# Optimization experiments

Hardware: AMD Instinct MI355X
Metric: run time of the kernel (lower is better)

## Reference

```python
import jax, jax.numpy as jnp
import numpy as np

N_HEADS = 8
N_HIDDEN = 64  # out_features // n_heads
SLOPE = 0.2
NEG = -9e15


def setup_inputs() -> dict:
    key = jax.random.key(0)
    k1, k2, k3, k4, k5 = jax.random.split(key, 5)
    B, N, F_in, F_out = 4, 2048, 512, 512
    h = jax.random.normal(k1, (B, N, F_in), dtype=jnp.float32)
    adj = jax.random.randint(k2, (B, N, N), 0, 2, dtype=jnp.int32)
    # xavier_uniform with gain=1.414: limit = gain*sqrt(6/(fan_in+fan_out))
    lim_W = 1.414 * np.sqrt(6.0 / (F_in + F_out))
    W_l = jax.random.uniform(k3, (F_in, F_out), jnp.float32, -lim_W, lim_W)
    W_r = jax.random.uniform(k4, (F_in, F_out), jnp.float32, -lim_W, lim_W)
    lim_a = 1.414 * np.sqrt(6.0 / (N_HIDDEN + 1))
    a = jax.random.uniform(k5, (N_HIDDEN, 1), jnp.float32, -lim_a, lim_a)
    return {"h": h, "adj": adj, "W_l": W_l, "W_r": W_r, "a": a}


def reference(h, adj, W_l, W_r, a):
    B, N, _ = h.shape
    H, d = N_HEADS, N_HIDDEN
    # torch .view(-1, H, N, d) is a raw row-major reshape, replicated exactly here
    Wh_l = jax.nn.leaky_relu((h @ W_l).reshape(B, H, N, d), SLOPE)
    Wh_r = jax.nn.leaky_relu((h @ W_r).reshape(B, H, N, d), SLOPE)
    # e: [B,H,N,1] + [B,H,1,N] -> [B,H,N,N]
    e = Wh_l @ a + jnp.swapaxes(Wh_r @ a, 2, 3)
    att = jnp.where(adj[:, None, :, :] > 0, e, NEG)
    att = jax.nn.softmax(att, axis=-1)
    h_prime = att @ Wh_r  # [B,H,N,d]
    # torch .view(-1, N, H*d): raw reshape (no head transpose)
    out = jax.nn.elu(h_prime.reshape(B, N, H * d))
    return out
```

## Files before the change

kernel.cpp:

```cpp
#include <hip/hip_runtime.h>

#define NB   4
#define NN   2048
#define FIN  512
#define FOUT 512
#define NHD  8
#define DH   64
#define VC   576
#define SLOPE 0.2f

typedef __attribute__((ext_vector_type(8)))  short bhalf8;
typedef __attribute__((ext_vector_type(16))) float f32x16;

__device__ __forceinline__ void load_lds16(const void* g, void* l) {
  __builtin_amdgcn_global_load_lds(
      (const __attribute__((address_space(1))) unsigned int*)g,
      (__attribute__((address_space(3))) unsigned int*)l, 16, 0, 0);
}

__device__ __forceinline__ unsigned int bfpair(float lo, float hi) {
  unsigned int a = __float_as_uint(lo), b = __float_as_uint(hi);
  a = (a + 0x7FFFu + ((a >> 16) & 1u)) >> 16;
  b = (b + 0x7FFFu + ((b >> 16) & 1u)) & 0xFFFF0000u;
  return a | b;
}

__device__ __forceinline__ void split2(float x, float y,
                                       unsigned int& hp, unsigned int& lp) {
  unsigned int ux = __float_as_uint(x), uy = __float_as_uint(y);
  unsigned int rx = (ux + 0x7FFFu + ((ux >> 16) & 1u)) & 0xFFFF0000u;
  unsigned int ry = (uy + 0x7FFFu + ((uy >> 16) & 1u)) & 0xFFFF0000u;
  float lx = x - __uint_as_float(rx);
  float ly = y - __uint_as_float(ry);
  unsigned int vx = __float_as_uint(lx), vy = __float_as_uint(ly);
  hp = (rx >> 16) | ry;
  lp = ((vx + 0x7FFFu + ((vx >> 16) & 1u)) >> 16)
     | ((vy + 0x7FFFu + ((vy >> 16) & 1u)) & 0xFFFF0000u);
}

__global__ __launch_bounds__(256) void k_split_h(
    const float* __restrict__ h,
    unsigned short* __restrict__ hHi, unsigned short* __restrict__ hLo)
{
  size_t base = ((size_t)blockIdx.x * 256 + threadIdx.x) * 8;
  float4 a = *(const float4*)(h + base);
  float4 b = *(const float4*)(h + base + 4);
  uint4 uh, ul;
  split2(a.x, a.y, uh.x, ul.x);
  split2(a.z, a.w, uh.y, ul.y);
  split2(b.x, b.y, uh.z, ul.z);
  split2(b.z, b.w, uh.w, ul.w);
  *(uint4*)(hHi + base) = uh;
  *(uint4*)(hLo + base) = ul;
}

__global__ __launch_bounds__(256) void k_prep_wr(
    const float* __restrict__ Wr,
    unsigned short* __restrict__ wTh, unsigned short* __restrict__ wTl)
{
  __shared__ float s[64][65];
  const int t = threadIdx.x;
  const int k0 = blockIdx.y * 64, n0 = blockIdx.x * 64;
#pragma unroll
  for (int p = 0; p < 4; ++p) {
    int row = p * 16 + (t >> 4);
    int col = (t & 15) * 4;
    float4 v = *(const float4*)(Wr + (size_t)(k0 + row) * FOUT + n0 + col);
    s[row][col] = v.x; s[row][col+1] = v.y; s[row][col+2] = v.z; s[row][col+3] = v.w;
  }
  __syncthreads();
  const int n = t >> 2;
  const int ks = (t & 3) * 16;
  uint4 h0, h1, l0, l1;
  split2(s[ks+ 0][n], s[ks+ 1][n], h0.x, l0.x);
  split2(s[ks+ 2][n], s[ks+ 3][n], h0.y, l0.y);
  split2(s[ks+ 4][n], s[ks+ 5][n], h0.z, l0.z);
  split2(s[ks+ 6][n], s[ks+ 7][n], h0.w, l0.w);
  split2(s[ks+ 8][n], s[ks+ 9][n], h1.x, l1.x);
  split2(s[ks+10][n], s[ks+11][n], h1.y, l1.y);
  split2(s[ks+12][n], s[ks+13][n], h1.z, l1.z);
  split2(s[ks+14][n], s[ks+15][n], h1.w, l1.w);
  size_t o = (size_t)(n0 + n) * FIN + k0 + ks;
  *(uint4*)(wTh + o) = h0; *(uint4*)(wTh + o + 8) = h1;
  *(uint4*)(wTl + o) = l0; *(uint4*)(wTl + o + 8) = l1;
}

__global__ __launch_bounds__(256) void k_gemm_whr_mfma(
    const unsigned short* __restrict__ hHi, const unsigned short* __restrict__ hLo,
    const unsigned short* __restrict__ wTh, const unsigned short* __restrict__ wTl,
    float* __restrict__ Whr)
{
  __shared__ unsigned short sAh[128*64], sAl[128*64];
  __shared__ unsigned short sBh[64*64],  sBl[64*64];
  const int tid = threadIdx.x, lane = tid & 63, wv = tid >> 6;
  const int Bid = blockIdx.x;
  const int g8 = Bid & 7, idx = Bid >> 3;
  const int sg = idx >> 3, ct = idx & 7;
  const int c0 = ct * 64;
  const int row0 = (g8 * 8 + sg) * 128;

  const unsigned short* pAh[4]; const unsigned short* pAl[4];
  unsigned short *dAh[4], *dAl[4];
#pragma unroll
  for (int t = 0; t < 4; ++t) {
    int I  = wv + t * 4;
    int rl = I * 8 + (lane >> 3);
    int gk = (lane & 7) ^ (rl & 7);
    pAh[t] = hHi + (size_t)(row0 + rl) * FIN + gk * 8;
    pAl[t] = hLo + (size_t)(row0 + rl) * FIN + gk * 8;
    dAh[t] = sAh + I * 512;  dAl[t] = sAl + I * 512;
  }
  const unsigned short* pBh[2]; const unsigned short* pBl[2];
  unsigned short *dBh[2], *dBl[2];
#pragma unroll
  for (int t = 0; t < 2; ++t) {
    int I  = wv + t * 4;
    int rl = I * 8 + (lane >> 3);
    int gk = (lane & 7) ^ (rl & 7);
    pBh[t] = wTh + (size_t)(c0 + rl) * FIN + gk * 8;
    pBl[t] = wTl + (size_t)(c0 + rl) * FIN + gk * 8;
    dBh[t] = sBh + I * 512;  dBl[t] = sBl + I * 512;
  }

  const int wi = wv >> 1, wc = wv & 1;
  const int l31 = lane & 31, half = lane >> 5;
  const int aoff0 = (wi*64 +      l31) * 64;
  const int aoff1 = (wi*64 + 32 + l31) * 64;
  const int boff  = (wc*32 +      l31) * 64;
  f32x16 acc0 = {}; f32x16 acc1 = {};

  for (int k0 = 0; k0 < FIN; k0 += 64) {
#pragma unroll
    for (int t = 0; t < 4; ++t) { load_lds16(pAh[t] + k0, dAh[t]);
                                  load_lds16(pAl[t] + k0, dAl[t]); }
#pragma unroll
    for (int t = 0; t < 2; ++t) { load_lds16(pBh[t] + k0, dBh[t]);
                                  load_lds16(pBl[t] + k0, dBl[t]); }
    __syncthreads();
#pragma unroll
    for (int kb = 0; kb < 4; ++kb) {
      int kg = ((kb*2 + half) ^ (lane & 7)) * 8;
      bhalf8 bh  = *(const bhalf8*)&sBh[boff  + kg];
      bhalf8 bl  = *(const bhalf8*)&sBl[boff  + kg];
      bhalf8 a0h = *(const bhalf8*)&sAh[aoff0 + kg];
      bhalf8 a0l = *(const bhalf8*)&sAl[aoff0 + kg];
      bhalf8 a1h = *(const bhalf8*)&sAh[aoff1 + kg];
      bhalf8 a1l = *(const bhalf8*)&sAl[aoff1 + kg];
      acc0 = __builtin_amdgcn_mfma_f32_32x32x16_bf16(a0h, bh, acc0, 0, 0, 0);
      acc1 = __builtin_amdgcn_mfma_f32_32x32x16_bf16(a1h, bh, acc1, 0, 0, 0);
      acc0 = __builtin_amdgcn_mfma_f32_32x32x16_bf16(a0l, bh, acc0, 0, 0, 0);
      acc1 = __builtin_amdgcn_mfma_f32_32x32x16_bf16(a1l, bh, acc1, 0, 0, 0);
      acc0 = __builtin_amdgcn_mfma_f32_32x32x16_bf16(a0h, bl, acc0, 0, 0, 0);
      acc1 = __builtin_amdgcn_mfma_f32_32x32x16_bf16(a1h, bl, acc1, 0, 0, 0);
    }
    __syncthreads();
  }

  const int colb = c0 + wc*32 + l31;
#pragma unroll
  for (int mi = 0; mi < 2; ++mi) {
    const f32x16 a = mi ? acc1 : acc0;
#pragma unroll
    for (int reg = 0; reg < 16; ++reg) {
      int grow = row0 + wi*64 + mi*32 + ((reg & 3) + 8*(reg >> 2) + 4*half);
      int b  = grow >> 11;
      int n  = grow & 2047;
      int hd = n >> 8;
      int jj = ((n & 255) << 3) | ct;
      int dd = colb & 63;
      float v = a[reg];
      v = v > 0.f ? v : SLOPE * v;
      Whr[(((size_t)(b*NHD + hd)) * NN + jj) * DH + dd] = v;
    }
  }
}

__global__ __launch_bounds__(256) void k_er(
    const float* __restrict__ Whr, const float* __restrict__ av,
    float* __restrict__ er)
{
  int gtid = blockIdx.x * 256 + threadIdx.x;
  int row  = gtid >> 6;
  int lane = threadIdx.x & 63;
  float v = Whr[(size_t)row * DH + lane] * av[lane];
#pragma unroll
  for (int off = 32; off; off >>= 1) v += __shfl_down(v, off, 64);
  if (lane == 0) er[row] = v;
}

__global__ __launch_bounds__(256) void k_softmax_w(float* __restrict__ er)
{
  __shared__ float wm[4];
  float* p = er + (size_t)blockIdx.x * NN;
  float m = -1e30f;
  for (int j = threadIdx.x; j < NN; j += 256) m = fmaxf(m, p[j]);
#pragma unroll
  for (int off = 32; off; off >>= 1) m = fmaxf(m, __shfl_down(m, off, 64));
  if ((threadIdx.x & 63) == 0) wm[threadIdx.x >> 6] = m;
  __syncthreads();
  float mm = fmaxf(fmaxf(wm[0], wm[1]), fmaxf(wm[2], wm[3]));
  for (int j = threadIdx.x; j < NN; j += 256) p[j] = expf(p[j] - mm);
}

__global__ __launch_bounds__(256) void k_build_vt(
    const float* __restrict__ Whr, const float* __restrict__ w,
    unsigned short* __restrict__ Vt)
{
  const int lane = threadIdx.x & 63, wv = threadIdx.x >> 6;
  const int c = blockIdx.y * 4 + wv;
  const int b = blockIdx.z;
  const int j = blockIdx.x * 512 + lane * 8;
  uint4 o = {0u, 0u, 0u, 0u};
  if (c < 512) {
    const int hh = c >> 6, dd = c & 63;
    const size_t r = ((size_t)(b*NHD + hh))*NN + j;
    const float* wp = w + r;
    const float* hp = Whr + r*DH + dd;
    float v[8];
#pragma unroll
    for (int q = 0; q < 8; ++q) v[q] = wp[q] * hp[(size_t)q*DH];
    o.x = bfpair(v[0], v[1]); o.y = bfpair(v[2], v[3]);
    o.z = bfpair(v[4], v[5]); o.w = bfpair(v[6], v[7]);
  } else if (c < 520) {
    const size_t r = ((size_t)(b*NHD + (c - 512)))*NN + j;
    float4 a0 = *(const float4*)(w + r);
    float4 a1 = *(const float4*)(w + r + 4);
    o.x = bfpair(a0.x, a0.y); o.y = bfpair(a0.z, a0.w);
    o.z = bfpair(a1.x, a1.y); o.w = bfpair(a1.z, a1.w);
  }
  *(uint4*)(Vt + ((size_t)(b*VC + c))*NN + j) = o;
}

__global__ __launch_bounds__(256) void k_attn_mfma(
    const int* __restrict__ adj, const unsigned short* __restrict__ Vt,
    float* __restrict__ C)
{
  __shared__ unsigned short sA[128][72];
  __shared__ unsigned short sB[64][64];
  const int tid = threadIdx.x;
  const int lane = tid & 63, wv = tid >> 6;
  const int Bid = blockIdx.x;
  const int g8 = Bid & 7, idx = Bid >> 3;
  const int ct = idx >> 3, sg = idx & 7;
  const int c0 = ct * 64;
  const int row0 = (g8 * 8 + sg) * 128;
  const int b = row0 >> 11;

  const unsigned short* pB[2];
  unsigned short* dB[2];
#pragma unroll
  for (int t = 0; t < 2; ++t) {
    int I  = wv + t*4;
    int rl = I*8 + (lane >> 3);
    int gk = (lane & 7) ^ (rl & 7);
    pB[t] = Vt + ((size_t)(b*VC + c0 + rl))*NN + gk*8;
    dB[t] = &sB[0][0] + I*512;
  }
  const int* adjp = adj + (size_t)b*NN*NN + (size_t)(row0 & 2047)*NN
                    + (tid >> 3)*NN + (tid & 7)*8;
  unsigned short* sAp = &sA[tid >> 3][(tid & 7)*8];

  const int wi = wv >> 1, wc = wv & 1;
  const int l31 = lane & 31, half = lane >> 5;
  f32x16 acc0 = {}; f32x16 acc1 = {};
  const unsigned short* aRd0 = &sA[wi*64 +      l31][half*8];
  const unsigned short* aRd1 = &sA[wi*64 + 32 + l31][half*8];
  const int nloc = wc*32 + l31;

  for (int k0 = 0; k0 < NN; k0 += 64) {
    load_lds16(pB[0] + k0, dB[0]);
    load_lds16(pB[1] + k0, dB[1]);
#pragma unroll
    for (int rr = 0; rr < 4; ++rr) {
      const int* p = adjp + rr*32*NN + k0;
      int4 q0 = *(const int4*)p;
      int4 q1 = *(const int4*)(p + 4);
      uint4 u;
      u.x = (unsigned)(q0.x | (q0.y << 16)) * 0x3F80u;
      u.y = (unsigned)(q0.z | (q0.w << 16)) * 0x3F80u;
      u.z = (unsigned)(q1.x | (q1.y << 16)) * 0x3F80u;
      u.w = (unsigned)(q1.z | (q1.w << 16)) * 0x3F80u;
      *(uint4*)(sAp + rr*32*72) = u;
    }
    __syncthreads();
#pragma unroll
    for (int kb = 0; kb < 4; ++kb) {
      int kg = (kb*2 + half) ^ (lane & 7);
      bhalf8 bf = *(const bhalf8*)&sB[nloc][kg*8];
      bhalf8 a0 = *(const bhalf8*)(aRd0 + kb*16);
      bhalf8 a1 = *(const bhalf8*)(aRd1 + kb*16);
      acc0 = __builtin_amdgcn_mfma_f32_32x32x16_bf16(a0, bf, acc0, 0, 0, 0);
      acc1 = __builtin_amdgcn_mfma_f32_32x32x16_bf16(a1, bf, acc1, 0, 0, 0);
    }
    __syncthreads();
  }
  float* Cp = C + ((size_t)(row0 + wi*64))*VC + c0 + wc*32 + l31;
#pragma unroll
  for (int mi = 0; mi < 2; ++mi) {
    const f32x16 a = mi ? acc1 : acc0;
#pragma unroll
    for (int reg = 0; reg < 16; ++reg) {
      int irow = (reg & 3) + 8*(reg >> 2) + 4*half + mi*32;
      Cp[(size_t)irow * VC] = a[reg];
    }
  }
}

__global__ __launch_bounds__(256) void k_epilogue(
    const float* __restrict__ C, float* __restrict__ out)
{
  int idx = blockIdx.x * 256 + threadIdx.x;
  int d  = idx & 63;
  int t  = idx >> 6;
  int hh = t & 7;
  int bi = t >> 3;
  int i  = bi & 2047, b = bi >> 11;
  float num = C[(size_t)bi * VC + (hh << 6) + d];
  float den = C[(size_t)bi * VC + 512 + hh];
  float v = num / den;
  v = v > 0.f ? v : expm1f(v);
  int n = (hh << 8) | (i >> 3);
  int f = ((i & 7) << 6) | d;
  out[((size_t)b * NN + n) * FOUT + f] = v;
}

extern "C" void kernel_launch(void* const* d_in, const int* in_sizes, int n_in,
                              void* d_out, int out_size, void* d_ws, size_t ws_size,
                              hipStream_t stream)
{
  const float* hin = (const float*)d_in[0];
  const int*   adj = (const int*)d_in[1];
  const float* Wr  = (const float*)d_in[3];
  const float* av  = (const float*)d_in[4];
  float* out = (float*)d_out;

  char* ws = (char*)d_ws;
  unsigned short* hHi = (unsigned short*)(ws);
  unsigned short* hLo = (unsigned short*)(ws + 8388608);
  unsigned short* wTh = (unsigned short*)(ws + 16777216);
  unsigned short* wTl = (unsigned short*)(ws + 17301504);
  float* Whr  = (float*)(ws + 17825792);
  float* wexp = (float*)(ws + 34603008);
  unsigned short* Vt = (unsigned short*)(ws);
  float* C    = (float*)(ws + 17825792);

  k_split_h      <<<dim3(2048),           256, 0, stream>>>(hin, hHi, hLo);
  k_prep_wr      <<<dim3(8, 8),           256, 0, stream>>>(Wr, wTh, wTl);
  k_gemm_whr_mfma<<<dim3(512),            256, 0, stream>>>(hHi, hLo, wTh, wTl, Whr);
  k_er           <<<dim3(NB*NHD*NN/4),    256, 0, stream>>>(Whr, av, wexp);
  k_softmax_w    <<<dim3(NB*NHD),         256, 0, stream>>>(wexp);
  k_build_vt     <<<dim3(NN/512, VC/4, NB), 256, 0, stream>>>(Whr, wexp, Vt);
  k_attn_mfma    <<<dim3(9*64),           256, 0, stream>>>(adj, Vt, C);
  k_epilogue     <<<dim3(NB*NN*FOUT/256), 256, 0, stream>>>(C, out);
}
```

Before: 220.6 us.

## Fuse prep kernels, fold er reduction into GEMM, split-K attention with atomics

Merges the h-split and W_r-prep kernels into a single launch, and moves the er dot-product into the GEMM epilogue as a shuffle reduction followed by atomic adds, which removes the separate k_er pass that re-read Whr. The attention MFMA kernel is split in two along K, doubling the block count for better CU occupancy, and partial results are combined with atomic adds into C. Both atomic paths need memsets, which add extra traffic and make the float summation order nondeterministic.

```diff
diff --git a/kernel.cpp b/kernel.cpp
--- a/kernel.cpp
+++ b/kernel.cpp
@@ -38,29 +38,29 @@
      | ((vy + 0x7FFFu + ((vy >> 16) & 1u)) & 0xFFFF0000u);
 }
 
-__global__ __launch_bounds__(256) void k_split_h(
+__global__ __launch_bounds__(256) void k_split_prep(
     const float* __restrict__ h,
-    unsigned short* __restrict__ hHi, unsigned short* __restrict__ hLo)
-{
-  size_t base = ((size_t)blockIdx.x * 256 + threadIdx.x) * 8;
-  float4 a = *(const float4*)(h + base);
-  float4 b = *(const float4*)(h + base + 4);
-  uint4 uh, ul;
-  split2(a.x, a.y, uh.x, ul.x);
-  split2(a.z, a.w, uh.y, ul.y);
-  split2(b.x, b.y, uh.z, ul.z);
-  split2(b.z, b.w, uh.w, ul.w);
-  *(uint4*)(hHi + base) = uh;
-  *(uint4*)(hLo + base) = ul;
-}
-
-__global__ __launch_bounds__(256) void k_prep_wr(
+    unsigned short* __restrict__ hHi, unsigned short* __restrict__ hLo,
     const float* __restrict__ Wr,
     unsigned short* __restrict__ wTh, unsigned short* __restrict__ wTl)
 {
   __shared__ float s[64][65];
   const int t = threadIdx.x;
-  const int k0 = blockIdx.y * 64, n0 = blockIdx.x * 64;
+  if (blockIdx.x < 2048) {
+    size_t base = ((size_t)blockIdx.x * 256 + t) * 8;
+    float4 a = *(const float4*)(h + base);
+    float4 b = *(const float4*)(h + base + 4);
+    uint4 uh, ul;
+    split2(a.x, a.y, uh.x, ul.x);
+    split2(a.z, a.w, uh.y, ul.y);
+    split2(b.x, b.y, uh.z, ul.z);
+    split2(b.z, b.w, uh.w, ul.w);
+    *(uint4*)(hHi + base) = uh;
+    *(uint4*)(hLo + base) = ul;
+    return;
+  }
+  const int bid2 = blockIdx.x - 2048;
+  const int n0 = (bid2 & 7) * 64, k0 = (bid2 >> 3) * 64;
 #pragma unroll
   for (int p = 0; p < 4; ++p) {
     int row = p * 16 + (t >> 4);
@@ -88,7 +88,7 @@
 __global__ __launch_bounds__(256) void k_gemm_whr_mfma(
     const unsigned short* __restrict__ hHi, const unsigned short* __restrict__ hLo,
     const unsigned short* __restrict__ wTh, const unsigned short* __restrict__ wTl,
-    float* __restrict__ Whr)
+    float* __restrict__ Whr, const float* __restrict__ av, float* __restrict__ er)
 {
   __shared__ unsigned short sAh[128*64], sAl[128*64];
   __shared__ unsigned short sBh[64*64],  sBl[64*64];
@@ -156,7 +156,7 @@
     __syncthreads();
   }
 
-  const int colb = c0 + wc*32 + l31;
+  const float a_d = av[wc*32 + l31];
 #pragma unroll
   for (int mi = 0; mi < 2; ++mi) {
     const f32x16 a = mi ? acc1 : acc0;
@@ -167,25 +167,20 @@
       int n  = grow & 2047;
       int hd = n >> 8;
       int jj = ((n & 255) << 3) | ct;
-      int dd = colb & 63;
+      int dd = wc*32 + l31;
       float v = a[reg];
       v = v > 0.f ? v : SLOPE * v;
       Whr[(((size_t)(b*NHD + hd)) * NN + jj) * DH + dd] = v;
-    }
-  }
-}
-
-__global__ __launch_bounds__(256) void k_er(
-    const float* __restrict__ Whr, const float* __restrict__ av,
-    float* __restrict__ er)
-{
-  int gtid = blockIdx.x * 256 + threadIdx.x;
-  int row  = gtid >> 6;
-  int lane = threadIdx.x & 63;
-  float v = Whr[(size_t)row * DH + lane] * av[lane];
-#pragma unroll
-  for (int off = 32; off; off >>= 1) v += __shfl_down(v, off, 64);
-  if (lane == 0) er[row] = v;
+      float p = v * a_d;
+      p += __shfl_xor(p, 16, 32);
+      p += __shfl_xor(p,  8, 32);
+      p += __shfl_xor(p,  4, 32);
+      p += __shfl_xor(p,  2, 32);
+      p += __shfl_xor(p,  1, 32);
+      if (l31 == 0)
+        unsafeAtomicAdd(er + ((size_t)(b*NHD + hd)) * NN + jj, p);
+    }
+  }
 }
 
 __global__ __launch_bounds__(256) void k_softmax_w(float* __restrict__ er)
@@ -240,7 +235,9 @@
   const int tid = threadIdx.x;
   const int lane = tid & 63, wv = tid >> 6;
   const int Bid = blockIdx.x;
-  const int g8 = Bid & 7, idx = Bid >> 3;
+  const int g8 = Bid & 7;
+  const int kh = (Bid >> 3) & 1;
+  const int idx = Bid >> 4;
   const int ct = idx >> 3, sg = idx & 7;
   const int c0 = ct * 64;
   const int row0 = (g8 * 8 + sg) * 128;
@@ -267,7 +264,8 @@
   const unsigned short* aRd1 = &sA[wi*64 + 32 + l31][half*8];
   const int nloc = wc*32 + l31;
 
-  for (int k0 = 0; k0 < NN; k0 += 64) {
+  const int kbeg = kh * 1024, kend = kbeg + 1024;
+  for (int k0 = kbeg; k0 < kend; k0 += 64) {
     load_lds16(pB[0] + k0, dB[0]);
     load_lds16(pB[1] + k0, dB[1]);
 #pragma unroll
@@ -301,7 +299,7 @@
 #pragma unroll
     for (int reg = 0; reg < 16; ++reg) {
       int irow = (reg & 3) + 8*(reg >> 2) + 4*half + mi*32;
-      Cp[(size_t)irow * VC] = a[reg];
+      unsafeAtomicAdd(Cp + (size_t)irow * VC, a[reg]);
     }
   }
 }
@@ -344,12 +342,12 @@
   unsigned short* Vt = (unsigned short*)(ws);
   float* C    = (float*)(ws + 17825792);
 
-  k_split_h      <<<dim3(2048),           256, 0, stream>>>(hin, hHi, hLo);
-  k_prep_wr      <<<dim3(8, 8),           256, 0, stream>>>(Wr, wTh, wTl);
-  k_gemm_whr_mfma<<<dim3(512),            256, 0, stream>>>(hHi, hLo, wTh, wTl, Whr);
-  k_er           <<<dim3(NB*NHD*NN/4),    256, 0, stream>>>(Whr, av, wexp);
+  hipMemsetAsync(wexp, 0, (size_t)NB*NHD*NN*4, stream);
+  k_split_prep   <<<dim3(2112),           256, 0, stream>>>(hin, hHi, hLo, Wr, wTh, wTl);
+  k_gemm_whr_mfma<<<dim3(512),            256, 0, stream>>>(hHi, hLo, wTh, wTl, Whr, av, wexp);
   k_softmax_w    <<<dim3(NB*NHD),         256, 0, stream>>>(wexp);
   k_build_vt     <<<dim3(NN/512, VC/4, NB), 256, 0, stream>>>(Whr, wexp, Vt);
-  k_attn_mfma    <<<dim3(9*64),           256, 0, stream>>>(adj, Vt, C);
+  hipMemsetAsync(C, 0, (size_t)NB*NN*VC*4, stream);
+  k_attn_mfma    <<<dim3(1152),           256, 0, stream>>>(adj, Vt, C);
   k_epilogue     <<<dim3(NB*NN*FOUT/256), 256, 0, stream>>>(C, out);
 }
```

Measured after the change: 237.8 us. 7.8% more time.
